# Optimization experiments

Measured on AMD Instinct MI355X. Metric: run time of the kernel, lower is better.

The kernel has to match this reference:

```python
import jax, jax.numpy as jnp
import numpy as np

B, L, D, H = 2, 2048, 2048, 16
DH = D // H  # 128 per-head dim
EPS = 1e-5


def setup_inputs() -> dict:
    key = jax.random.key(0)
    ks = jax.random.split(key, 6)
    s = 0.02  # xavier-ish init scale with gain 2**-2.5
    return {
        "hidden_states": jax.random.normal(ks[0], (B, L, D), jnp.float32),
        "Wq": jax.random.normal(ks[1], (D, D), jnp.float32) * s,
        "Wk": jax.random.normal(ks[2], (D, D), jnp.float32) * s,
        "Wv": jax.random.normal(ks[3], (D, D), jnp.float32) * s,
        "Wb": jax.random.normal(ks[4], (D, H), jnp.float32) * s,
        "o_norm_weight": jnp.ones((DH,), jnp.float32),
        "Wo": jax.random.normal(ks[5], (D, D), jnp.float32) * s,
    }


def _delta_rule(q, k, v, beta):
    """Recurrent delta-rule linear attention.
    q,k,v: [B,H,L,Dh]; beta: [B,H,L]. Math identical to fused_chunk_delta_rule.
    S_t = S_{t-1} + k_t (beta_t * (v_t - S_{t-1}^T k_t))^T ;  o_t = S_t^T q_t
    """
    def step(S, inp):
        qt, kt, vt, bt = inp  # [B,H,Dh],[B,H,Dh],[B,H,Dh],[B,H]
        v_pred = jnp.einsum('bhk,bhkv->bhv', kt, S)
        delta = (vt - v_pred) * bt[..., None]
        S = S + kt[..., None] * delta[:, :, None, :]
        ot = jnp.einsum('bhk,bhkv->bhv', qt, S)
        return S, ot

    xs = (q.transpose(2, 0, 1, 3), k.transpose(2, 0, 1, 3),
          v.transpose(2, 0, 1, 3), beta.transpose(2, 0, 1))
    S0 = jnp.zeros(q.shape[:2] + (q.shape[-1], v.shape[-1]), q.dtype)
    _, o = jax.lax.scan(step, S0, xs)  # o: [L,B,H,Dh]
    return o.transpose(1, 2, 0, 3)  # [B,H,L,Dh]


def reference(hidden_states, Wq, Wk, Wv, Wb, o_norm_weight, Wo):
    b, l, d = hidden_states.shape
    h = Wb.shape[1]
    dh = d // h

    q = hidden_states @ Wq
    k = hidden_states @ Wk
    v = jax.nn.silu(hidden_states @ Wv)

    def heads(x):
        return x.reshape(b, l, h, dh).transpose(0, 2, 1, 3)  # b h l d

    q, k, v = heads(q), heads(k), heads(v)

    # qk_norm = 'l2' (torch F.normalize with eps clamp)
    def l2n(x):
        n = jnp.sqrt(jnp.sum(x * x, axis=-1, keepdims=True))
        return x / jnp.maximum(n, 1e-12)

    q, k = l2n(q), l2n(k)
    q = q * (dh ** -0.5)  # fla delta-rule default scale

    beta = jax.nn.sigmoid(hidden_states @ Wb).transpose(0, 2, 1)  # b h l

    o = _delta_rule(q, k, v, beta)  # b h l dh
    o = o.transpose(0, 2, 1, 3)  # b l h dh

    # RMSNorm over head_v_dim
    o = o * jax.lax.rsqrt(jnp.mean(o * o, axis=-1, keepdims=True) + EPS)
    o = o * o_norm_weight

    return o.reshape(b, l, d) @ Wo
```

## Files before the change

### kernel.cpp

```cpp
#include <hip/hip_runtime.h>
#include <hip/hip_bf16.h>
#include <cstdint>

#define DEV static __device__ __forceinline__

typedef unsigned short u16;
typedef unsigned int u32;
typedef __attribute__((ext_vector_type(8))) short short8;
typedef __attribute__((ext_vector_type(4))) float f32x4;

constexpr int Bn = 2, Ln = 2048, Dn = 2048, Hn = 16;
constexpr int Mrows = Bn * Ln;
constexpr int CHK = 64, NCK = Ln / CHK;
constexpr int NCHUNKS = Bn * Hn * NCK;

DEV float b2f(u16 s) { union { float f; u32 u; } x; x.u = ((u32)s) << 16; return x.f; }
DEV u16 f2b(float f) {
  union { float f; u32 u; } x; x.f = f; u32 u = x.u;
  return (u16)((u + 0x7fffu + ((u >> 16) & 1u)) >> 16);
}

DEV void cp16(const void* g, void* l) {
  __builtin_amdgcn_global_load_lds(
      (const __attribute__((address_space(1))) u32*)(unsigned long long)(g),
      (__attribute__((address_space(3))) u32*)(unsigned long long)(l), 16, 0, 0);
}

DEV f32x4 mfma16(short8 a, short8 b, f32x4 c) {
  return __builtin_amdgcn_mfma_f32_16x16x32_bf16(a, b, c, 0, 0, 0);
}

__global__ void k_cvt(const float* __restrict__ src, u16* __restrict__ dst, int n8) {
  int i = blockIdx.x * blockDim.x + threadIdx.x;
  if (i >= n8) return;
  const float4* s4 = (const float4*)(src + (size_t)i * 8);
  float4 a = s4[0], b = s4[1];
  u16 o[8] = {f2b(a.x), f2b(a.y), f2b(a.z), f2b(a.w), f2b(b.x), f2b(b.y), f2b(b.z), f2b(b.w)};
  *(short8*)(dst + (size_t)i * 8) = *(short8*)o;
}

struct TransArgs {
  const float* src[5]; u16* dst[5]; int rows[5]; int cols[5];
};
__global__ void k_trans(TransArgs t) {
  __shared__ u16 tile[32][33];
  int z = blockIdx.z;
  const float* src = t.src[z]; u16* dst = t.dst[z];
  int rows = t.rows[z], cols = t.cols[z];
  int r0 = blockIdx.y * 32, c0 = blockIdx.x * 32;
  if (r0 >= rows || c0 >= cols) return;
  int tx = threadIdx.x, ty = threadIdx.y;
  for (int i = ty; i < 32; i += 8) {
    int r = r0 + i, c = c0 + tx;
    if (r < rows && c < cols) tile[i][tx] = f2b(src[(size_t)r * cols + c]);
  }
  __syncthreads();
  for (int i = ty; i < 32; i += 8) {
    int r = c0 + i, c = r0 + tx;
    if (r < cols && c < rows) dst[(size_t)r * rows + c] = tile[tx][i];
  }
}

__global__ __launch_bounds__(256) void k_beta(const u16* __restrict__ hs,
                                              const u16* __restrict__ WbT,
                                              float* __restrict__ beta_g) {
  int tid = threadIdx.x, wave = tid >> 6, lane = tid & 63, quad = lane >> 4, l15 = lane & 15;
  int tok0 = blockIdx.x * 64 + wave * 16;
  const u16* arow = hs + (size_t)(tok0 + l15) * Dn;
  const u16* brow = WbT + (size_t)l15 * Dn;
  f32x4 acc = {0.f, 0.f, 0.f, 0.f};
  for (int k = 0; k < Dn; k += 32) {
    short8 af = *(const short8*)&arow[k + quad * 8];
    short8 bf = *(const short8*)&brow[k + quad * 8];
    acc = mfma16(af, bf, acc);
  }
  int b = (blockIdx.x * 64) >> 11;
  int l = (blockIdx.x * 64 + wave * 16) & 2047;
#pragma unroll
  for (int r = 0; r < 4; r++) {
    beta_g[(size_t)(b * Hn + l15) * Ln + l + quad * 4 + r] = 1.f / (1.f + __expf(-acc[r]));
  }
}

struct GemmArgs {
  const u16* A; const u16* Bt; void* C; int epi;
  int f32out;
  int M, N, K;
};
__global__ __launch_bounds__(256) void k_gemm(GemmArgs g) {
  __shared__ u16 As[128 * 64];
  __shared__ u16 Bs[128 * 64];
  const u16* A = g.A; const u16* Bt = g.Bt;
  int epi = g.epi;
  int K = g.K, N = g.N;
  int tid = threadIdx.x, wave = tid >> 6, lane = tid & 63;
  int quad = lane >> 4, l15 = lane & 15;
  int m0 = blockIdx.y * 128, n0 = blockIdx.x * 128;
  int wm = (wave >> 1) * 64, wn = (wave & 1) * 64;
  f32x4 acc[4][4];
#pragma unroll
  for (int i = 0; i < 4; i++)
#pragma unroll
    for (int j = 0; j < 4; j++) acc[i][j] = (f32x4){0.f, 0.f, 0.f, 0.f};
  const u16* Ag = A + (size_t)(m0 + wave * 32 + (lane >> 3)) * K + (lane & 7) * 8;
  const u16* Bg = Bt + (size_t)(n0 + wave * 32 + (lane >> 3)) * K + (lane & 7) * 8;
  u16* Al = &As[wave * 32 * 64];
  u16* Bl = &Bs[wave * 32 * 64];
  for (int k0 = 0; k0 < K; k0 += 64) {
#pragma unroll
    for (int t = 0; t < 4; t++) {
      cp16(Ag + k0 + t * 8 * K, Al + t * 8 * 64);
      cp16(Bg + k0 + t * 8 * K, Bl + t * 8 * 64);
    }
    __syncthreads();
#pragma unroll
    for (int kk = 0; kk < 64; kk += 32) {
      short8 af[4], bf[4];
#pragma unroll
      for (int i = 0; i < 4; i++) af[i] = *(const short8*)&As[(wm + i * 16 + l15) * 64 + kk + quad * 8];
#pragma unroll
      for (int i = 0; i < 4; i++) bf[i] = *(const short8*)&Bs[(wn + i * 16 + l15) * 64 + kk + quad * 8];
#pragma unroll
      for (int i = 0; i < 4; i++)
#pragma unroll
        for (int j = 0; j < 4; j++) acc[i][j] = mfma16(af[i], bf[j], acc[i][j]);
    }
    __syncthreads();
  }
#pragma unroll
  for (int i = 0; i < 4; i++)
#pragma unroll
    for (int j = 0; j < 4; j++) {
      int row = m0 + wm + i * 16 + quad * 4;
      int col = n0 + wn + j * 16 + l15;
#pragma unroll
      for (int r = 0; r < 4; r++) {
        float v = acc[i][j][r];
        if (epi == 1) v = v / (1.f + __expf(-v));
        if (g.f32out) ((float*)g.C)[(size_t)(row + r) * N + col] = v;
        else ((u16*)g.C)[(size_t)(row + r) * N + col] = f2b(v);
      }
    }
}

struct Gemm2Args { const u16* A; const u16* Bt; u16* C; int K; };

DEV const short8* fragp(const u16* buf, int row, int colb) {
  return (const short8*)((const char*)buf + row * 128 + (colb ^ ((row & 4) << 3)));
}

__global__ __launch_bounds__(512, 2) void k_gemm2(Gemm2Args g) {
  __shared__ u16 lds[2][2][256 * 64];
  const int K = g.K, NT = K / 64;
  const size_t Kb = (size_t)K * 2;
  int tid = threadIdx.x, wave = tid >> 6, lane = tid & 63;
  int quad = lane >> 4, l15 = lane & 15;
  int wm = wave >> 2, wn = wave & 3;

  int bid = blockIdx.x;
  int wg = (bid & 7) * 48 + (bid >> 3);
  int by = wg / 24, bx = wg - by * 24;
  int m0 = by * 256, n0f = bx * 256;

  const char* gA0 = (const char*)g.A + (size_t)(m0 + wave * 8 + (lane >> 3)) * Kb +
                    (((lane & 7) * 16) ^ (lane & 32));
  const char* gB0 = (const char*)g.Bt + (size_t)(n0f + wave * 8 + (lane >> 3)) * Kb +
                    (((lane & 7) * 16) ^ (lane & 32));

  auto stage = [&](int buf, int t) {
    const char* pa = gA0 + (size_t)t * 128;
    const char* pb = gB0 + (size_t)t * 128;
    u16* la = &lds[buf][0][wave * 512];
    u16* lb = &lds[buf][1][wave * 512];
#pragma unroll
    for (int s = 0; s < 4; s++) {
      cp16(pa + (size_t)s * 64 * Kb, la + s * 4096);
      cp16(pb + (size_t)s * 64 * Kb, lb + s * 4096);
    }
  };

  f32x4 acc0[4][4], acc1[4][4];
#pragma unroll
  for (int i = 0; i < 4; i++)
#pragma unroll
    for (int j = 0; j < 4; j++) {
      acc0[i][j] = (f32x4){0.f, 0.f, 0.f, 0.f};
      acc1[i][j] = (f32x4){0.f, 0.f, 0.f, 0.f};
    }

  int ra = wm * 128 + l15;
  int rb = wn * 64 + l15;
  int cb0 = quad * 16;
  int cb1 = 64 + quad * 16;

  stage(0, 0);
  stage(1, 1);

  for (int t = 0; t < NT; ++t) {
    int cur = t & 1;
    if (t == NT - 1) {
      asm volatile("s_waitcnt vmcnt(0)" ::: "memory");
    } else {
      asm volatile("s_waitcnt vmcnt(8)" ::: "memory");
    }
    __builtin_amdgcn_s_barrier();
    __builtin_amdgcn_sched_barrier(0);
    const u16* bA = &lds[cur][0][0];
    const u16* bB = &lds[cur][1][0];

    short8 A0[4], A1[4], B0[4];
#pragma unroll
    for (int i = 0; i < 4; i++) A0[i] = *fragp(bA, ra + i * 16, cb0);
#pragma unroll
    for (int j = 0; j < 4; j++) B0[j] = *fragp(bB, rb + j * 16, cb0);
    __builtin_amdgcn_s_setprio(1);
#pragma unroll
    for (int i = 0; i < 4; i++)
#pragma unroll
      for (int j = 0; j < 4; j++) acc0[i][j] = mfma16(A0[i], B0[j], acc0[i][j]);
    __builtin_amdgcn_s_setprio(0);
#pragma unroll
    for (int i = 0; i < 4; i++) A1[i] = *fragp(bA, ra + 64 + i * 16, cb0);
    __builtin_amdgcn_s_setprio(1);
#pragma unroll
    for (int i = 0; i < 4; i++)
#pragma unroll
      for (int j = 0; j < 4; j++) acc1[i][j] = mfma16(A1[i], B0[j], acc1[i][j]);
    __builtin_amdgcn_s_setprio(0);
#pragma unroll
    for (int i = 0; i < 4; i++) A0[i] = *fragp(bA, ra + i * 16, cb1);
#pragma unroll
    for (int j = 0; j < 4; j++) B0[j] = *fragp(bB, rb + j * 16, cb1);
    __builtin_amdgcn_s_setprio(1);
#pragma unroll
    for (int i = 0; i < 4; i++)
#pragma unroll
      for (int j = 0; j < 4; j++) acc0[i][j] = mfma16(A0[i], B0[j], acc0[i][j]);
    __builtin_amdgcn_s_setprio(0);
#pragma unroll
    for (int i = 0; i < 4; i++) A1[i] = *fragp(bA, ra + 64 + i * 16, cb1);
    __builtin_amdgcn_s_setprio(1);
#pragma unroll
    for (int i = 0; i < 4; i++)
#pragma unroll
      for (int j = 0; j < 4; j++) acc1[i][j] = mfma16(A1[i], B0[j], acc1[i][j]);
    __builtin_amdgcn_s_setprio(0);

    __builtin_amdgcn_s_barrier();
    if (t + 2 < NT) stage(cur, t + 2);
  }

  int zq = n0f >> 11;
  u16* Cz = g.C + (size_t)zq * ((size_t)Mrows * 2048);
  int colB = (n0f & 2047) + wn * 64;
  int rowB = m0 + wm * 128;
#pragma unroll
  for (int mq = 0; mq < 2; mq++) {
#pragma unroll
    for (int i = 0; i < 4; i++)
#pragma unroll
      for (int j = 0; j < 4; j++) {
        f32x4 a = mq ? acc1[i][j] : acc0[i][j];
        int row = rowB + mq * 64 + i * 16 + quad * 4;
        int col = colB + j * 16 + l15;
#pragma unroll
        for (int r = 0; r < 4; r++) {
          float v = a[r];
          if (zq == 2) v = v / (1.f + __expf(-v));
          Cz[(size_t)(row + r) * 2048 + col] = f2b(v);
        }
      }
  }
}

__global__ void k_l2(u16* qn, u16* kn) {
  int tid = threadIdx.x, wave = tid >> 6, lane = tid & 63;
  size_t row = (size_t)blockIdx.x * 4 + wave;
  u16* p = (blockIdx.y ? kn : qn) + row * 128;
  u32 u = *(const u32*)&p[lane * 2];
  float x0 = b2f((u16)(u & 0xffff)), x1 = b2f((u16)(u >> 16));
  float ss = x0 * x0 + x1 * x1;
#pragma unroll
  for (int o = 32; o > 0; o >>= 1) ss += __shfl_xor(ss, o, 64);
  float sc = 1.f / fmaxf(sqrtf(ss), 1e-12f);
  if (blockIdx.y == 0) sc *= 0.08838834764831845f;
  u32 outv = (u32)f2b(x0 * sc) | ((u32)f2b(x1 * sc) << 16);
  *(u32*)&p[lane * 2] = outv;
}

constexpr int ST = 72;
__global__ __launch_bounds__(256, 4) void k_pre(
    const float* __restrict__ beta_g,
    const u16* __restrict__ qn, const u16* __restrict__ kn, const u16* __restrict__ vn,
    u16* __restrict__ W2g, u16* __restrict__ Ug, u16* __restrict__ Gg, u16* __restrict__ KTg) {
  __shared__ float beta_s[64];
  __shared__ u16 mats[4 * 64 * ST];
  int gid = blockIdx.x;
  int c = gid & 31, h = (gid >> 5) & 15, b = gid >> 9;
  int tid = threadIdx.x;
  int l0 = c * 64;

  if (tid < 64) beta_s[tid] = beta_g[(size_t)(b * Hn + h) * Ln + l0 + tid];
  __syncthreads();

  int wave = tid >> 6, lane = tid & 63, quad = lane >> 4, l15 = lane & 15;
  u16 *Br = mats, *Bc = mats + 64 * ST, *M0 = mats + 2 * 64 * ST, *M1 = mats + 3 * 64 * ST;

  {
    const u16* krowB = kn + (size_t)(b * Ln + l0 + wave * 16 + l15) * Dn + h * 128;
    short8 bfr[4];
#pragma unroll
    for (int s = 0; s < 4; s++) bfr[s] = *(const short8*)&krowB[quad * 8 + 32 * s];
#pragma unroll
    for (int mt = 0; mt < 4; ++mt) {
      const u16* arow_k = kn + (size_t)(b * Ln + l0 + mt * 16 + l15) * Dn + h * 128;
      const u16* arow_q = qn + (size_t)(b * Ln + l0 + mt * 16 + l15) * Dn + h * 128;
      f32x4 accA = {0.f, 0.f, 0.f, 0.f}, accG = {0.f, 0.f, 0.f, 0.f};
#pragma unroll
      for (int s = 0; s < 4; s++) {
        short8 ak = *(const short8*)&arow_k[quad * 8 + 32 * s];
        short8 aq = *(const short8*)&arow_q[quad * 8 + 32 * s];
        accA = mfma16(ak, bfr[s], accA);
        accG = mfma16(aq, bfr[s], accG);
      }
      int t = wave * 16 + l15;
#pragma unroll
      for (int r = 0; r < 4; r++) {
        int i = mt * 16 + quad * 4 + r;
        u16 nb = f2b((t < i) ? -beta_s[i] * accA[r] : 0.f);
        Br[i * ST + t] = nb;
        Bc[t * ST + i] = nb;
        M0[i * ST + t] = (t == i) ? f2b(1.f) : nb;
        Gg[(size_t)gid * 4096 + (size_t)i * 64 + t] = f2b((t <= i) ? accG[r] : 0.f);
      }
    }
  }
  __syncthreads();

  u16 *Mc = M0, *Mn = M1;
#pragma unroll
  for (int it = 0; it < 5; ++it) {
    const int tT = (it < 3) ? 0 : ((it == 3) ? 1 : 2);
    const int tI = (it < 4) ? 0 : 1;
    short8 bb[2];
#pragma unroll
    for (int s = 0; s < 2; s++) bb[s] = *(const short8*)&Bc[(wave * 16 + l15) * ST + quad * 8 + 32 * s];
    f32x4 accT[4];
#pragma unroll
    for (int mt = 0; mt < 4; mt++) {
      accT[mt] = (f32x4){0.f, 0.f, 0.f, 0.f};
      if (mt - wave >= tT) {
#pragma unroll
        for (int s = 0; s < 2; s++) {
          short8 af = *(const short8*)&Br[(mt * 16 + l15) * ST + quad * 8 + 32 * s];
          accT[mt] = mfma16(af, bb[s], accT[mt]);
        }
      }
    }
    __syncthreads();
#pragma unroll
    for (int mt = 0; mt < 4; mt++) {
      if (mt - wave >= tI) {
#pragma unroll
        for (int r = 0; r < 4; r++) {
          int i = mt * 16 + quad * 4 + r, t = wave * 16 + l15;
          u16 v = f2b(accT[mt][r]);
          Br[i * ST + t] = v;
          Bc[t * ST + i] = v;
        }
      }
    }
    __syncthreads();
    short8 tb[2];
#pragma unroll
    for (int s = 0; s < 2; s++) tb[s] = *(const short8*)&Bc[(wave * 16 + l15) * ST + quad * 8 + 32 * s];
#pragma unroll
    for (int mt = 0; mt < 4; mt++) {
      if (mt - wave >= tT) {
        f32x4 a;
#pragma unroll
        for (int r = 0; r < 4; r++) a[r] = b2f(Mc[(mt * 16 + quad * 4 + r) * ST + wave * 16 + l15]);
#pragma unroll
        for (int s = 0; s < 2; s++) {
          short8 af = *(const short8*)&Mc[(mt * 16 + l15) * ST + quad * 8 + 32 * s];
          a = mfma16(af, tb[s], a);
        }
#pragma unroll
        for (int r = 0; r < 4; r++) Mn[(mt * 16 + quad * 4 + r) * ST + wave * 16 + l15] = f2b(a[r]);
      } else {
#pragma unroll
        for (int r = 0; r < 4; r++)
          Mn[(mt * 16 + quad * 4 + r) * ST + wave * 16 + l15] =
              Mc[(mt * 16 + quad * 4 + r) * ST + wave * 16 + l15];
      }
    }
    u16* tmp = Mc; Mc = Mn; Mn = tmp;
  }
  __syncthreads();

  u16* XT = mats;
  for (int pass = 0; pass < 2; ++pass) {
    const u16* src = pass ? vn : kn;
    for (int idx = tid; idx < 64 * 128; idx += 256) {
      int t = idx >> 7, dk = idx & 127;
      float v = b2f(src[(size_t)(b * Ln + l0 + t) * Dn + h * 128 + dk]);
      XT[dk * ST + t] = f2b(v * beta_s[t]);
      if (pass == 0) KTg[(size_t)gid * 8192 + (size_t)dk * 64 + t] = f2b(v);
    }
    __syncthreads();
    u16* dst = pass ? Ug : W2g;
#pragma unroll
    for (int half = 0; half < 2; ++half) {
      int nt = wave + half * 4;
      short8 bx[2];
#pragma unroll
      for (int s = 0; s < 2; s++) bx[s] = *(const short8*)&XT[(nt * 16 + l15) * ST + quad * 8 + 32 * s];
#pragma unroll
      for (int mt = 0; mt < 4; mt++) {
        f32x4 a = {0.f, 0.f, 0.f, 0.f};
#pragma unroll
        for (int s = 0; s < 2; s++) {
          short8 af = *(const short8*)&Mc[(mt * 16 + l15) * ST + quad * 8 + 32 * s];
          a = mfma16(af, bx[s], a);
        }
#pragma unroll
        for (int r = 0; r < 4; r++)
          dst[(size_t)gid * 8192 + (size_t)(mt * 16 + quad * 4 + r) * 128 + nt * 16 + l15] = f2b(a[r]);
      }
    }
    __syncthreads();
  }
}

struct Frg { short8 w2[4], qf[4], gf[2], k0[2], k1[2]; float u[4]; };

__global__ __launch_bounds__(256) void k_scan(
    const u16* __restrict__ qn, const u16* __restrict__ W2g, const u16* __restrict__ Ug,
    const u16* __restrict__ Gg, const u16* __restrict__ KTg, u16* __restrict__ Og) {
  constexpr int SST = 136, DST = 104;
  __shared__ u16 Sb[16 * SST];
  __shared__ u16 Db[16 * DST];
  int bh = blockIdx.x, sl = blockIdx.y;
  int b = bh >> 4, h = bh & 15, c0 = sl * 16;
  int tid = threadIdx.x, wave = tid >> 6, lane = tid & 63, quad = lane >> 4, l15 = lane & 15;
  for (int i = tid; i < 16 * SST; i += 256) Sb[i] = 0;
  f32x4 accS0 = {0.f, 0.f, 0.f, 0.f}, accS1 = {0.f, 0.f, 0.f, 0.f};
  __syncthreads();

  auto load_frags = [&](Frg& F, int ci) {
    size_t ck = (size_t)bh * NCK + ci;
    const u16* w2row = W2g + ck * 8192 + (size_t)(wave * 16 + l15) * 128;
    const u16* qrow = qn + (size_t)(b * Ln + ci * 64 + wave * 16 + l15) * Dn + h * 128;
#pragma unroll
    for (int s = 0; s < 4; s++) {
      F.w2[s] = *(const short8*)&w2row[quad * 8 + 32 * s];
      F.qf[s] = *(const short8*)&qrow[quad * 8 + 32 * s];
    }
    const u16* grow = Gg + ck * 4096 + (size_t)(wave * 16 + l15) * 64;
    const u16* kt0 = KTg + ck * 8192 + (size_t)(wave * 16 + l15) * 64;
    const u16* kt1 = KTg + ck * 8192 + (size_t)((wave + 4) * 16 + l15) * 64;
#pragma unroll
    for (int s = 0; s < 2; s++) {
      F.gf[s] = *(const short8*)&grow[quad * 8 + 32 * s];
      F.k0[s] = *(const short8*)&kt0[quad * 8 + 32 * s];
      F.k1[s] = *(const short8*)&kt1[quad * 8 + 32 * s];
    }
    const u16* urow = Ug + ck * 8192 + (size_t)(wave * 16 + quad * 4) * 128 + c0 + l15;
#pragma unroll
    for (int r = 0; r < 4; r++) F.u[r] = b2f(urow[(size_t)r * 128]);
  };

  auto compute = [&](const Frg& F, int ci) {
    f32x4 accT = {0.f, 0.f, 0.f, 0.f}, accO = {0.f, 0.f, 0.f, 0.f};
#pragma unroll
    for (int s = 0; s < 4; s++) {
      short8 sf = *(const short8*)&Sb[l15 * SST + quad * 8 + 32 * s];
      accT = mfma16(F.w2[s], sf, accT);
      accO = mfma16(F.qf[s], sf, accO);
    }
#pragma unroll
    for (int r = 0; r < 4; r++) {
      float d = F.u[r] - accT[r];
      Db[l15 * DST + wave * 16 + quad * 4 + r] = f2b(d);
    }
    __syncthreads();
#pragma unroll
    for (int s = 0; s < 2; s++) {
      short8 df = *(const short8*)&Db[l15 * DST + quad * 8 + 32 * s];
      accO = mfma16(F.gf[s], df, accO);
      accS0 = mfma16(F.k0[s], df, accS0);
      accS1 = mfma16(F.k1[s], df, accS1);
    }
    u16* orow = Og + (size_t)(b * Ln + ci * 64 + wave * 16 + quad * 4) * Dn + h * 128 + c0 + l15;
#pragma unroll
    for (int r = 0; r < 4; r++) orow[(size_t)r * Dn] = f2b(accO[r]);
#pragma unroll
    for (int r = 0; r < 4; r++) {
      Sb[l15 * SST + wave * 16 + quad * 4 + r] = f2b(accS0[r]);
      Sb[l15 * SST + (wave + 4) * 16 + quad * 4 + r] = f2b(accS1[r]);
    }
    __syncthreads();
  };

  Frg FA, FB;
  load_frags(FA, 0);
  for (int ci = 0; ci < NCK; ci += 2) {
    load_frags(FB, ci + 1);
    compute(FA, ci);
    if (ci + 2 < NCK) load_frags(FA, ci + 2);
    compute(FB, ci + 1);
  }
}

__global__ void k_rms(const u16* __restrict__ Og, const float* __restrict__ w, u16* __restrict__ out) {
  int tid = threadIdx.x, wave = tid >> 6, lane = tid & 63;
  size_t row = (size_t)blockIdx.x * 4 + wave;
  const u16* p = Og + row * 128;
  u32 u = *(const u32*)&p[lane * 2];
  float x0 = b2f((u16)(u & 0xffff)), x1 = b2f((u16)(u >> 16));
  float ss = x0 * x0 + x1 * x1;
#pragma unroll
  for (int o = 32; o > 0; o >>= 1) ss += __shfl_xor(ss, o, 64);
  float sc = rsqrtf(ss * (1.f / 128.f) + 1e-5f);
  float w0 = w[lane * 2], w1 = w[lane * 2 + 1];
  u32 o2 = (u32)f2b(x0 * sc * w0) | ((u32)f2b(x1 * sc * w1) << 16);
  *(u32*)&out[row * 128 + lane * 2] = o2;
}

extern "C" void kernel_launch(void* const* d_in, const int* in_sizes, int n_in,
                              void* d_out, int out_size, void* d_ws, size_t ws_size,
                              hipStream_t stream) {
  (void)in_sizes; (void)n_in; (void)out_size; (void)ws_size;
  const float* hs_f = (const float*)d_in[0];
  const float* Wq = (const float*)d_in[1];
  const float* Wk = (const float*)d_in[2];
  const float* Wv = (const float*)d_in[3];
  const float* Wb = (const float*)d_in[4];
  const float* onw = (const float*)d_in[5];
  const float* Wo = (const float*)d_in[6];

  char* ws = (char*)d_ws;
  size_t off = 0;
  auto alloc = [&](size_t bytes) -> void* {
    void* p = ws + off;
    off += (bytes + 255) & ~(size_t)255;
    return p;
  };
  const size_t WB = (size_t)2048 * 2048 * 2;
  const size_t XB = (size_t)4096 * 2048 * 2;
  u16* WqT = (u16*)alloc(WB);
  u16* WkT = (u16*)alloc(WB);
  u16* WvT = (u16*)alloc(WB);
  u16* WoT = (u16*)alloc(WB);
  u16* WbT = (u16*)alloc((size_t)16 * 2048 * 2);
  u16* hsb = (u16*)alloc(XB);
  u16* qn  = (u16*)alloc(XB);
  u16* kn  = (u16*)alloc(XB);
  u16* vn  = (u16*)alloc(XB);
  u16* W2g = (u16*)alloc((size_t)NCHUNKS * 8192 * 2);
  u16* Ug  = (u16*)alloc((size_t)NCHUNKS * 8192 * 2);
  u16* Gg  = (u16*)alloc((size_t)NCHUNKS * 4096 * 2);
  u16* KTg = (u16*)alloc((size_t)NCHUNKS * 8192 * 2);
  float* beta_g = (float*)alloc((size_t)Bn * Hn * Ln * 4);
  u16* Og = vn;
  u16* onorm = qn;

  hipLaunchKernelGGL(k_cvt, dim3(Mrows * Dn / 8 / 256), dim3(256), 0, stream, hs_f, hsb, Mrows * Dn / 8);

  TransArgs ta;
  ta.src[0] = Wq; ta.dst[0] = WqT; ta.rows[0] = 2048; ta.cols[0] = 2048;
  ta.src[1] = Wk; ta.dst[1] = WkT; ta.rows[1] = 2048; ta.cols[1] = 2048;
  ta.src[2] = Wv; ta.dst[2] = WvT; ta.rows[2] = 2048; ta.cols[2] = 2048;
  ta.src[3] = Wo; ta.dst[3] = WoT; ta.rows[3] = 2048; ta.cols[3] = 2048;
  ta.src[4] = Wb; ta.dst[4] = WbT; ta.rows[4] = 2048; ta.cols[4] = 16;
  hipLaunchKernelGGL(k_trans, dim3(64, 64, 5), dim3(32, 8), 0, stream, ta);

  hipLaunchKernelGGL(k_beta, dim3(Mrows / 64), dim3(256), 0, stream, hsb, WbT, beta_g);

  {
    Gemm2Args g2;
    g2.A = hsb; g2.Bt = WqT; g2.C = qn; g2.K = 2048;
    hipLaunchKernelGGL(k_gemm2, dim3(384), dim3(512), 0, stream, g2);
  }

  hipLaunchKernelGGL(k_l2, dim3(16384, 2), dim3(256), 0, stream, qn, kn);

  hipLaunchKernelGGL(k_pre, dim3(NCHUNKS), dim3(256), 0, stream,
                     beta_g, qn, kn, vn, W2g, Ug, Gg, KTg);

  hipLaunchKernelGGL(k_scan, dim3(32, 8), dim3(256), 0, stream,
                     qn, W2g, Ug, Gg, KTg, Og);

  hipLaunchKernelGGL(k_rms, dim3(16384), dim3(256), 0, stream, Og, onw, onorm);

  GemmArgs go;
  go.A = onorm; go.Bt = WoT; go.C = d_out; go.epi = 0;
  go.f32out = 1; go.M = Mrows; go.N = 2048; go.K = 2048;
  hipLaunchKernelGGL(k_gemm, dim3(16, 32), dim3(256), 0, stream, go);
}
```

Baseline: 510.0 us.

## Widen fused QKV GEMM tile to 256x384 with triple-buffered half-K LDS pipeline

The fused QKV projection GEMM now uses 256x384 output tiles, giving 256 blocks instead of 384, which matches the 256 CUs, with 4x6 MFMA fragments per wave. The LDS plan moves from a double-buffered full-K-step staging to a three-slot ring of 32-wide K halves, with finer waits and barriers so loads overlap compute. The goal is a single full wave of blocks, more reuse per loaded tile, and less tail imbalance. The cost is the removal of the XOR swizzle, which may cause LDS bank conflicts, plus higher register pressure and more barriers per iteration.

```diff
diff --git a/kernel.cpp b/kernel.cpp
--- a/kernel.cpp
+++ b/kernel.cpp
@@ -145,12 +145,9 @@
 
 struct Gemm2Args { const u16* A; const u16* Bt; u16* C; int K; };
 
-DEV const short8* fragp(const u16* buf, int row, int colb) {
-  return (const short8*)((const char*)buf + row * 128 + (colb ^ ((row & 4) << 3)));
-}
-
 __global__ __launch_bounds__(512, 2) void k_gemm2(Gemm2Args g) {
-  __shared__ u16 lds[2][2][256 * 64];
+  __shared__ u16 ldsbuf[61440];
+  const char* LB = (const char*)ldsbuf;
   const int K = g.K, NT = K / 64;
   const size_t Kb = (size_t)K * 2;
   int tid = threadIdx.x, wave = tid >> 6, lane = tid & 63;
@@ -158,115 +155,145 @@
   int wm = wave >> 2, wn = wave & 3;
 
   int bid = blockIdx.x;
-  int wg = (bid & 7) * 48 + (bid >> 3);
-  int by = wg / 24, bx = wg - by * 24;
-  int m0 = by * 256, n0f = bx * 256;
-
-  const char* gA0 = (const char*)g.A + (size_t)(m0 + wave * 8 + (lane >> 3)) * Kb +
-                    (((lane & 7) * 16) ^ (lane & 32));
-  const char* gB0 = (const char*)g.Bt + (size_t)(n0f + wave * 8 + (lane >> 3)) * Kb +
-                    (((lane & 7) * 16) ^ (lane & 32));
-
-  auto stage = [&](int buf, int t) {
-    const char* pa = gA0 + (size_t)t * 128;
-    const char* pb = gB0 + (size_t)t * 128;
-    u16* la = &lds[buf][0][wave * 512];
-    u16* lb = &lds[buf][1][wave * 512];
-#pragma unroll
-    for (int s = 0; s < 4; s++) {
-      cp16(pa + (size_t)s * 64 * Kb, la + s * 4096);
-      cp16(pb + (size_t)s * 64 * Kb, lb + s * 4096);
-    }
+  int wg = (bid & 7) * 32 + (bid >> 3);
+  int by = wg >> 4, bx = wg & 15;
+  int m0 = by * 256, n0f = bx * 384;
+
+  int r0 = tid >> 2;
+  int cby = (tid & 3) * 16;
+  const char* gA = (const char*)g.A + (size_t)(m0 + r0) * Kb + cby;
+  const char* gB = (const char*)g.Bt + (size_t)(n0f + r0) * Kb + cby;
+
+  auto stageA = [&](int slot, int t, int kh) {
+    const char* src = gA + (size_t)t * 128 + kh * 64;
+    u16* dst = &ldsbuf[slot * 8192 + tid * 8];
+    cp16(src, dst);
+    cp16(src + (size_t)128 * Kb, dst + 4096);
   };
-
-  f32x4 acc0[4][4], acc1[4][4];
+  auto stageB = [&](int slot, int t, int kh) {
+    const char* src = gB + (size_t)t * 128 + kh * 64;
+    u16* dst = &ldsbuf[24576 + slot * 12288 + tid * 8];
+    cp16(src, dst);
+    cp16(src + (size_t)128 * Kb, dst + 4096);
+    cp16(src + (size_t)256 * Kb, dst + 8192);
+  };
+
+  f32x4 acc0[4][6], acc1[4][6];
 #pragma unroll
   for (int i = 0; i < 4; i++)
 #pragma unroll
-    for (int j = 0; j < 4; j++) {
+    for (int j = 0; j < 6; j++) {
       acc0[i][j] = (f32x4){0.f, 0.f, 0.f, 0.f};
       acc1[i][j] = (f32x4){0.f, 0.f, 0.f, 0.f};
     }
 
-  int ra = wm * 128 + l15;
-  int rb = wn * 64 + l15;
-  int cb0 = quad * 16;
-  int cb1 = 64 + quad * 16;
-
-  stage(0, 0);
-  stage(1, 1);
-
+  int rA = (wm * 128 + l15) * 64 + quad * 16;
+  int rB = (wn * 96 + l15) * 64 + quad * 16;
+
+  stageA(0, 0, 0);
+  stageB(0, 0, 0);
+  stageA(1, 0, 1);
+  stageB(1, 0, 1);
+
+  short8 bf[6];
+  int u0 = 0;
   for (int t = 0; t < NT; ++t) {
-    int cur = t & 1;
-    if (t == NT - 1) {
-      asm volatile("s_waitcnt vmcnt(0)" ::: "memory");
-    } else {
-      asm volatile("s_waitcnt vmcnt(8)" ::: "memory");
-    }
+    int u1 = u0 + 1; if (u1 == 3) u1 = 0;
+    int u2 = u1 + 1; if (u2 == 3) u2 = 0;
+    bool pf = (t + 1 < NT);
+    const char* aK0 = LB + u0 * 16384;
+    const char* aK1 = LB + u1 * 16384;
+    const char* bK0 = LB + 49152 + u0 * 24576;
+    const char* bK1 = LB + 49152 + u1 * 24576;
+
+    asm volatile("s_waitcnt vmcnt(5)" ::: "memory");
     __builtin_amdgcn_s_barrier();
     __builtin_amdgcn_sched_barrier(0);
-    const u16* bA = &lds[cur][0][0];
-    const u16* bB = &lds[cur][1][0];
-
-    short8 A0[4], A1[4], B0[4];
-#pragma unroll
-    for (int i = 0; i < 4; i++) A0[i] = *fragp(bA, ra + i * 16, cb0);
-#pragma unroll
-    for (int j = 0; j < 4; j++) B0[j] = *fragp(bB, rb + j * 16, cb0);
-    __builtin_amdgcn_s_setprio(1);
+    if (pf) stageA(u2, t + 1, 0);
+    {
+      short8 av[4];
+#pragma unroll
+      for (int i = 0; i < 4; i++) av[i] = *(const short8*)(aK0 + rA + i * 1024);
+#pragma unroll
+      for (int j = 0; j < 6; j++) bf[j] = *(const short8*)(bK0 + rB + j * 1024);
+      __builtin_amdgcn_s_setprio(1);
+#pragma unroll
+      for (int i = 0; i < 4; i++)
+#pragma unroll
+        for (int j = 0; j < 6; j++) acc0[i][j] = mfma16(av[i], bf[j], acc0[i][j]);
+      __builtin_amdgcn_s_setprio(0);
+    }
+
+    asm volatile("s_waitcnt vmcnt(5)" ::: "memory");
+    __builtin_amdgcn_s_barrier();
+    __builtin_amdgcn_sched_barrier(0);
+    if (pf) stageB(u2, t + 1, 0);
+    {
+      short8 av[4];
+#pragma unroll
+      for (int i = 0; i < 4; i++) av[i] = *(const short8*)(aK0 + rA + 4096 + i * 1024);
+      __builtin_amdgcn_s_setprio(1);
+#pragma unroll
+      for (int i = 0; i < 4; i++)
+#pragma unroll
+        for (int j = 0; j < 6; j++) acc1[i][j] = mfma16(av[i], bf[j], acc1[i][j]);
+      __builtin_amdgcn_s_setprio(0);
+    }
+
+    if (t == NT - 1) asm volatile("s_waitcnt vmcnt(0)" ::: "memory");
+    else asm volatile("s_waitcnt vmcnt(5)" ::: "memory");
+    __builtin_amdgcn_s_barrier();
+    __builtin_amdgcn_sched_barrier(0);
+    if (pf) stageA(u0, t + 1, 1);
+    {
+      short8 av[4];
+#pragma unroll
+      for (int i = 0; i < 4; i++) av[i] = *(const short8*)(aK1 + rA + i * 1024);
+#pragma unroll
+      for (int j = 0; j < 6; j++) bf[j] = *(const short8*)(bK1 + rB + j * 1024);
+      __builtin_amdgcn_s_setprio(1);
+#pragma unroll
+      for (int i = 0; i < 4; i++)
+#pragma unroll
+        for (int j = 0; j < 6; j++) acc0[i][j] = mfma16(av[i], bf[j], acc0[i][j]);
+      __builtin_amdgcn_s_setprio(0);
+    }
+
+    asm volatile("s_waitcnt vmcnt(5)" ::: "memory");
+    __builtin_amdgcn_s_barrier();
+    __builtin_amdgcn_sched_barrier(0);
+    if (pf) stageB(u0, t + 1, 1);
+    {
+      short8 av[4];
+#pragma unroll
+      for (int i = 0; i < 4; i++) av[i] = *(const short8*)(aK1 + rA + 4096 + i * 1024);
+      __builtin_amdgcn_s_setprio(1);
+#pragma unroll
+      for (int i = 0; i < 4; i++)
+#pragma unroll
+        for (int j = 0; j < 6; j++) acc1[i][j] = mfma16(av[i], bf[j], acc1[i][j]);
+      __builtin_amdgcn_s_setprio(0);
+    }
+
+    u0 = u2;
+  }
+
+#pragma unroll
+  for (int mq = 0; mq < 2; mq++) {
 #pragma unroll
     for (int i = 0; i < 4; i++)
 #pragma unroll
-      for (int j = 0; j < 4; j++) acc0[i][j] = mfma16(A0[i], B0[j], acc0[i][j]);
-    __builtin_amdgcn_s_setprio(0);
-#pragma unroll
-    for (int i = 0; i < 4; i++) A1[i] = *fragp(bA, ra + 64 + i * 16, cb0);
-    __builtin_amdgcn_s_setprio(1);
-#pragma unroll
-    for (int i = 0; i < 4; i++)
-#pragma unroll
-      for (int j = 0; j < 4; j++) acc1[i][j] = mfma16(A1[i], B0[j], acc1[i][j]);
-    __builtin_amdgcn_s_setprio(0);
-#pragma unroll
-    for (int i = 0; i < 4; i++) A0[i] = *fragp(bA, ra + i * 16, cb1);
-#pragma unroll
-    for (int j = 0; j < 4; j++) B0[j] = *fragp(bB, rb + j * 16, cb1);
-    __builtin_amdgcn_s_setprio(1);
-#pragma unroll
-    for (int i = 0; i < 4; i++)
-#pragma unroll
-      for (int j = 0; j < 4; j++) acc0[i][j] = mfma16(A0[i], B0[j], acc0[i][j]);
-    __builtin_amdgcn_s_setprio(0);
-#pragma unroll
-    for (int i = 0; i < 4; i++) A1[i] = *fragp(bA, ra + 64 + i * 16, cb1);
-    __builtin_amdgcn_s_setprio(1);
-#pragma unroll
-    for (int i = 0; i < 4; i++)
-#pragma unroll
-      for (int j = 0; j < 4; j++) acc1[i][j] = mfma16(A1[i], B0[j], acc1[i][j]);
-    __builtin_amdgcn_s_setprio(0);
-
-    __builtin_amdgcn_s_barrier();
-    if (t + 2 < NT) stage(cur, t + 2);
-  }
-
-  int zq = n0f >> 11;
-  u16* Cz = g.C + (size_t)zq * ((size_t)Mrows * 2048);
-  int colB = (n0f & 2047) + wn * 64;
-  int rowB = m0 + wm * 128;
-#pragma unroll
-  for (int mq = 0; mq < 2; mq++) {
-#pragma unroll
-    for (int i = 0; i < 4; i++)
-#pragma unroll
-      for (int j = 0; j < 4; j++) {
+      for (int j = 0; j < 6; j++) {
         f32x4 a = mq ? acc1[i][j] : acc0[i][j];
-        int row = rowB + mq * 64 + i * 16 + quad * 4;
-        int col = colB + j * 16 + l15;
+        int row = m0 + wm * 128 + mq * 64 + i * 16 + quad * 4;
+        int colg = n0f + wn * 96 + j * 16;
+        int z = colg >> 11;
+        u16* Cz = g.C + (size_t)z * ((size_t)Mrows * 2048);
+        int col = (colg & 2047) + l15;
 #pragma unroll
         for (int r = 0; r < 4; r++) {
           float v = a[r];
-          if (zq == 2) v = v / (1.f + __expf(-v));
+          if (z == 2) v = v / (1.f + __expf(-v));
           Cz[(size_t)(row + r) * 2048 + col] = f2b(v);
         }
       }
@@ -580,7 +607,7 @@
   {
     Gemm2Args g2;
     g2.A = hsb; g2.Bt = WqT; g2.C = qn; g2.K = 2048;
-    hipLaunchKernelGGL(k_gemm2, dim3(384), dim3(512), 0, stream, g2);
+    hipLaunchKernelGGL(k_gemm2, dim3(256), dim3(512), 0, stream, g2);
   }
 
   hipLaunchKernelGGL(k_l2, dim3(16384, 2), dim3(256), 0, stream, qn, kn);
```

Result: faster. 497.8 us (-2.4%).
